# Performance work log

Measured on AMD Instinct MI355X. Metric: run time of the kernel, lower is better.

## Reference

```python
import jax, jax.numpy as jnp
import numpy as np

GROUP_SIZE = 128

def setup_inputs() -> dict:
    key = jax.random.key(0)
    k1, k2, k3, k4, k5 = jax.random.split(key, 5)
    B, S, IN, OUT = 4, 2048, 4096, 4096
    G = IN // GROUP_SIZE  # 32 groups
    x = jax.random.normal(k1, (B, S, IN), dtype=jnp.float32)
    qweight = jax.random.randint(k2, (OUT, IN // 2), 0, 256, dtype=jnp.int32)
    scales = jax.random.uniform(k3, (OUT, G), dtype=jnp.float32) * 0.01 + 1e-4
    zeros = jax.random.randint(k4, (OUT, G), 0, 16, dtype=jnp.int32)
    bias = jax.random.normal(k5, (OUT,), dtype=jnp.float32) * 0.01
    return {"x": x, "qweight": qweight, "scales": scales, "zeros": zeros, "bias": bias}

def reference(x, qweight, scales, zeros, bias):
    out_f, half = qweight.shape
    in_f = half * 2
    G = scales.shape[1]
    # Unpack two 4-bit values per byte: low nibble at even index, high at odd.
    low = (qweight & 15).astype(x.dtype)
    high = ((qweight >> 4) & 15).astype(x.dtype)
    w = jnp.stack([low, high], axis=-1).reshape(out_f, in_f)  # interleaved [w0,w1,w2,...]
    # Groupwise dequant: (q - zero) * scale
    w = w.reshape(out_f, G, GROUP_SIZE)
    w = (w - zeros[:, :, None].astype(x.dtype)) * scales[:, :, None].astype(x.dtype)
    w = w.reshape(out_f, in_f)
    # Dense linear: y = x @ W^T + b
    out = jnp.einsum('bsi,oi->bso', x, w) + bias
    return out
```

## Files before the change

kernel.cpp:

```cpp
#include <hip/hip_runtime.h>
#include <hip/hip_bf16.h>

typedef __attribute__((ext_vector_type(4))) float f32x4;
typedef __attribute__((ext_vector_type(8))) short bf16x8;
typedef __attribute__((ext_vector_type(4))) int i32x4;

#define GS 128

#define GLOAD_LDS16(g, l)                                                        \
    __builtin_amdgcn_global_load_lds(                                            \
        (const __attribute__((address_space(1))) void*)(g),                      \
        (__attribute__((address_space(3))) void*)(l), 16, 0, 0)

__device__ __forceinline__ short f2bf(float f) {
    union { float f; unsigned u; } v; v.f = f;
    unsigned r = v.u + 0x7fffu + ((v.u >> 16) & 1u);
    return (short)(r >> 16);
}

__global__ void requant_w_kernel(const int* __restrict__ QW,
                                 const float* __restrict__ SC,
                                 const int* __restrict__ ZR,
                                 signed char* __restrict__ W8,
                                 float* __restrict__ WS, int K, int G) {
    const int o = blockIdx.x;
    const int tid = threadIdx.x;
    const int lane = tid & 63;
    const int wid = tid >> 6;
    const int g = tid / 8;
    const float s = SC[(long)o * G + g];
    const float z = (float)ZR[(long)o * G + g];
    const int* p = QW + (long)o * (K / 2) + tid * 8;
    int v[8];
#pragma unroll
    for (int j = 0; j < 8; ++j) v[j] = p[j];
    float w[16];
#pragma unroll
    for (int j = 0; j < 8; ++j) {
        w[2 * j]     = ((float)(v[j] & 15) - z) * s;
        w[2 * j + 1] = ((float)((v[j] >> 4) & 15) - z) * s;
    }
    float am = 0.f;
#pragma unroll
    for (int j = 0; j < 16; ++j) am = fmaxf(am, fabsf(w[j]));
#pragma unroll
    for (int off = 32; off >= 1; off >>= 1) am = fmaxf(am, __shfl_xor(am, off));
    __shared__ float red[4];
    if (lane == 0) red[wid] = am;
    __syncthreads();
    float wmax = fmaxf(fmaxf(red[0], red[1]), fmaxf(red[2], red[3]));
    wmax = fmaxf(wmax, 1e-30f);
    const float qs = 127.0f / wmax;
    int out[4];
#pragma unroll
    for (int j = 0; j < 4; ++j) {
        int b0 = ((int)rintf(w[4 * j]     * qs)) & 255;
        int b1 = ((int)rintf(w[4 * j + 1] * qs)) & 255;
        int b2 = ((int)rintf(w[4 * j + 2] * qs)) & 255;
        int b3 = ((int)rintf(w[4 * j + 3] * qs)) & 255;
        out[j] = b0 | (b1 << 8) | (b2 << 16) | (b3 << 24);
    }
    *(i32x4*)(W8 + (long)o * K + tid * 16) = *(i32x4*)out;
    if (tid == 0) WS[o] = wmax / 127.0f;
}

__global__ void quant_x_kernel(const float* __restrict__ X,
                               signed char* __restrict__ Xq,
                               float* __restrict__ XS, int K) {
    const int row = blockIdx.x;
    const int tid = threadIdx.x;
    const int lane = tid & 63;
    const int wid = tid >> 6;
    const float* px = X + (long)row * K + tid * 16;
    f32x4 v[4];
#pragma unroll
    for (int j = 0; j < 4; ++j) v[j] = *(const f32x4*)(px + j * 4);
    float am = 0.f;
#pragma unroll
    for (int j = 0; j < 4; ++j)
#pragma unroll
        for (int i = 0; i < 4; ++i) am = fmaxf(am, fabsf(v[j][i]));
#pragma unroll
    for (int off = 32; off >= 1; off >>= 1) am = fmaxf(am, __shfl_xor(am, off));
    __shared__ float red[4];
    if (lane == 0) red[wid] = am;
    __syncthreads();
    float amax = fmaxf(fmaxf(red[0], red[1]), fmaxf(red[2], red[3]));
    amax = fmaxf(amax, 1e-30f);
    const float qs = 127.0f / amax;
    int out[4];
#pragma unroll
    for (int j = 0; j < 4; ++j) {
        int b0 = ((int)rintf(v[j][0] * qs)) & 255;
        int b1 = ((int)rintf(v[j][1] * qs)) & 255;
        int b2 = ((int)rintf(v[j][2] * qs)) & 255;
        int b3 = ((int)rintf(v[j][3] * qs)) & 255;
        out[j] = b0 | (b1 << 8) | (b2 << 16) | (b3 << 24);
    }
    *(i32x4*)(Xq + (long)row * K + tid * 16) = *(i32x4*)out;
    if (tid == 0) XS[row] = amax / 127.0f;
}

__global__ __launch_bounds__(512, 2)
void gemm_i8_kernel(const signed char* __restrict__ A,
                    const signed char* __restrict__ B,
                    const float* __restrict__ WS,
                    const float* __restrict__ XS,
                    const float* __restrict__ BI,
                    float* __restrict__ Y,
                    int M, int N, int K) {
    extern __shared__ char smem[];

    const int tid = threadIdx.x;
    const int lane = tid & 63;
    const int wid = tid >> 6;
    const int wr = wid >> 2;
    const int wc = wid & 3;
    const int fr = lane & 15;
    const int fq = lane >> 4;

    const int nbn = N / 256;
    const int bid = blockIdx.x;
    const int cpx = gridDim.x >> 3;
    const int wgid = (bid & 7) * cpx + (bid >> 3);
    const int tm = wgid / nbn;
    const int tn = wgid % nbn;
    const long m0 = (long)tm * 256;
    const long n0 = (long)tn * 256;

    const int srow = wid * 8 + (lane >> 3);
    const int schunk = (lane & 7) ^ (lane >> 3);
    const signed char* gA = A + (m0 + srow) * (long)K + schunk * 16;
    const signed char* gB = B + (n0 + srow) * (long)K + schunk * 16;

    auto stageA = [&](int c, int i, int kt) {
        GLOAD_LDS16(gA + (long)i * 64 * K + (long)kt * 128,
                    smem + c * 65536 + i * 8192 + wid * 1024);
    };
    auto stageB = [&](int c, int i, int kt) {
        GLOAD_LDS16(gB + (long)i * 64 * K + (long)kt * 128,
                    smem + c * 65536 + 32768 + i * 8192 + wid * 1024);
    };

    const int rswz = fr & 7;

    i32x4 acc[8][4] = {};
    i32x4 bfr[4][2];
    i32x4 afr[2][2];

    const int NT = K / 128;

    stageB(0, 0, 0); stageB(0, 1, 0); stageB(0, 2, 0); stageB(0, 3, 0);
    stageA(0, 0, 0); stageA(0, 2, 0);
    stageA(0, 1, 0); stageA(0, 3, 0);
    asm volatile("s_waitcnt vmcnt(2)" ::: "memory");
    __builtin_amdgcn_s_barrier();

    for (int t = 0; t < NT - 1; ++t) {
        const int cur = t & 1;
        const char* sA = smem + cur * 65536;
        const char* sB = sA + 32768;
        const int nxt = cur ^ 1;
#pragma unroll
        for (int q = 0; q < 4; ++q) {
#pragma unroll
            for (int ml = 0; ml < 2; ++ml)
#pragma unroll
                for (int ks = 0; ks < 2; ++ks) {
                    int row = wr * 128 + (2 * q + ml) * 16 + fr;
                    afr[ml][ks] = *(const i32x4*)(sA + row * 128 + ((fq + 4 * ks) ^ rswz) * 16);
                }
            if (q == 0) {
#pragma unroll
                for (int nf = 0; nf < 4; ++nf)
#pragma unroll
                    for (int ks = 0; ks < 2; ++ks) {
                        int row = wc * 64 + nf * 16 + fr;
                        bfr[nf][ks] = *(const i32x4*)(sB + row * 128 + ((fq + 4 * ks) ^ rswz) * 16);
                    }
            }
            if (q == 0)      { stageB(nxt, 0, t + 1); stageB(nxt, 1, t + 1); }
            else if (q == 1) { stageB(nxt, 2, t + 1); stageB(nxt, 3, t + 1); }
            else if (q == 2) { stageA(nxt, 0, t + 1); stageA(nxt, 2, t + 1); }
            else             { stageA(nxt, 1, t + 1); stageA(nxt, 3, t + 1); }

            if (q == 0) asm volatile("s_waitcnt lgkmcnt(8)" ::: "memory");
            __builtin_amdgcn_s_barrier();
            __builtin_amdgcn_s_setprio(1);
#pragma unroll
            for (int ml = 0; ml < 2; ++ml)
#pragma unroll
                for (int nf = 0; nf < 4; ++nf)
                    acc[2 * q + ml][nf] = __builtin_amdgcn_mfma_i32_16x16x64_i8(
                        afr[ml][0], bfr[nf][0], acc[2 * q + ml][nf], 0, 0, 0);
#pragma unroll
            for (int ml = 0; ml < 2; ++ml)
#pragma unroll
                for (int nf = 0; nf < 4; ++nf)
                    acc[2 * q + ml][nf] = __builtin_amdgcn_mfma_i32_16x16x64_i8(
                        afr[ml][1], bfr[nf][1], acc[2 * q + ml][nf], 0, 0, 0);
            __builtin_amdgcn_s_setprio(0);
            if (q == 1) asm volatile("s_waitcnt vmcnt(4)" ::: "memory");
            if (q == 3) asm volatile("s_waitcnt vmcnt(2)" ::: "memory");
            __builtin_amdgcn_s_barrier();
        }
    }

    {
        const int cur = (NT - 1) & 1;
        const char* sA = smem + cur * 65536;
        const char* sB = sA + 32768;
#pragma unroll
        for (int q = 0; q < 4; ++q) {
#pragma unroll
            for (int ml = 0; ml < 2; ++ml)
#pragma unroll
                for (int ks = 0; ks < 2; ++ks) {
                    int row = wr * 128 + (2 * q + ml) * 16 + fr;
                    afr[ml][ks] = *(const i32x4*)(sA + row * 128 + ((fq + 4 * ks) ^ rswz) * 16);
                }
            if (q == 0) {
#pragma unroll
                for (int nf = 0; nf < 4; ++nf)
#pragma unroll
                    for (int ks = 0; ks < 2; ++ks) {
                        int row = wc * 64 + nf * 16 + fr;
                        bfr[nf][ks] = *(const i32x4*)(sB + row * 128 + ((fq + 4 * ks) ^ rswz) * 16);
                    }
            }
            __builtin_amdgcn_s_barrier();
            __builtin_amdgcn_s_setprio(1);
#pragma unroll
            for (int ml = 0; ml < 2; ++ml)
#pragma unroll
                for (int nf = 0; nf < 4; ++nf)
                    acc[2 * q + ml][nf] = __builtin_amdgcn_mfma_i32_16x16x64_i8(
                        afr[ml][0], bfr[nf][0], acc[2 * q + ml][nf], 0, 0, 0);
#pragma unroll
            for (int ml = 0; ml < 2; ++ml)
#pragma unroll
                for (int nf = 0; nf < 4; ++nf)
                    acc[2 * q + ml][nf] = __builtin_amdgcn_mfma_i32_16x16x64_i8(
                        afr[ml][1], bfr[nf][1], acc[2 * q + ml][nf], 0, 0, 0);
            __builtin_amdgcn_s_setprio(0);
            if (q == 1) asm volatile("s_waitcnt vmcnt(0)" ::: "memory");
            __builtin_amdgcn_s_barrier();
        }
    }

#pragma unroll
    for (int nf = 0; nf < 4; ++nf) {
        const long col = n0 + wc * 64 + nf * 16 + fr;
        const float ws = WS[col];
        const float bv = BI[col];
#pragma unroll
        for (int m = 0; m < 8; ++m) {
            const long rbase = m0 + wr * 128 + m * 16 + 4 * fq;
#pragma unroll
            for (int i = 0; i < 4; ++i)
                Y[(rbase + i) * N + col] =
                    (float)acc[m][nf][i] * (XS[rbase + i] * ws) + bv;
        }
    }
}

#define BM 128
#define BN 128
#define BK 64
#define PK 72

__global__ void gptq_gemm_fallback(const float* __restrict__ X,
                                   const int* __restrict__ QW,
                                   const float* __restrict__ SC,
                                   const int* __restrict__ ZR,
                                   const float* __restrict__ BI,
                                   float* __restrict__ Y,
                                   int M, int N, int K, int G) {
    __shared__ __align__(16) short As[BM * PK];
    __shared__ __align__(16) short Bs[BN * PK];

    const int tid = threadIdx.x;
    const int nbm = M / BM;
    const int bid = blockIdx.x;
    const int cpx = gridDim.x >> 3;
    const int wgid = (bid & 7) * cpx + (bid >> 3);
    const int tm = wgid % nbm;
    const int tn = wgid / nbm;
    const long m0 = (long)tm * BM;
    const long n0 = (long)tn * BN;
    const int Kp = K >> 1;

    const int lane = tid & 63;
    const int wid = tid >> 6;
    const int wr = wid >> 1;
    const int wc = wid & 1;
    const int fr = lane & 15;
    const int fq = lane >> 4;

    int srow[4], sq[4];
#pragma unroll
    for (int c = 0; c < 4; ++c) {
        int w = tid + 256 * c;
        srow[c] = w >> 3;
        sq[c] = w & 7;
    }

    f32x4 acc[4][4] = {};
    const int NT = K / BK;

    for (int kt = 0; kt < NT; ++kt) {
        const int g = (kt * BK) / GS;
        f32x4 a0[4], a1[4];
        i32x4 b4[4];
        float sc_r[4], zr_r[4];
#pragma unroll
        for (int c = 0; c < 4; ++c) {
            const float* pa = X + (m0 + srow[c]) * K + kt * BK + 8 * sq[c];
            a0[c] = *(const f32x4*)pa;
            a1[c] = *(const f32x4*)(pa + 4);
            const int* pb = QW + (n0 + srow[c]) * Kp + kt * (BK / 2) + 4 * sq[c];
            b4[c] = *(const i32x4*)pb;
            sc_r[c] = SC[(n0 + srow[c]) * G + g];
            zr_r[c] = (float)ZR[(n0 + srow[c]) * G + g];
        }
        __syncthreads();
#pragma unroll
        for (int c = 0; c < 4; ++c) {
            bf16x8 av;
#pragma unroll
            for (int i = 0; i < 4; ++i) av[i] = f2bf(a0[c][i]);
#pragma unroll
            for (int i = 0; i < 4; ++i) av[4 + i] = f2bf(a1[c][i]);
            *(bf16x8*)(As + srow[c] * PK + 8 * sq[c]) = av;
            bf16x8 bv;
#pragma unroll
            for (int j = 0; j < 4; ++j) {
                int v = b4[c][j];
                bv[2 * j]     = f2bf(((float)(v & 15) - zr_r[c]) * sc_r[c]);
                bv[2 * j + 1] = f2bf(((float)((v >> 4) & 15) - zr_r[c]) * sc_r[c]);
            }
            *(bf16x8*)(Bs + srow[c] * PK + 8 * sq[c]) = bv;
        }
        __syncthreads();
#pragma unroll
        for (int kk = 0; kk < BK; kk += 32) {
            bf16x8 a[4], b[4];
#pragma unroll
            for (int mf = 0; mf < 4; ++mf)
                a[mf] = *(const bf16x8*)(As + (wr * 64 + mf * 16 + fr) * PK + kk + 8 * fq);
#pragma unroll
            for (int nf = 0; nf < 4; ++nf)
                b[nf] = *(const bf16x8*)(Bs + (wc * 64 + nf * 16 + fr) * PK + kk + 8 * fq);
#pragma unroll
            for (int mf = 0; mf < 4; ++mf)
#pragma unroll
                for (int nf = 0; nf < 4; ++nf)
                    acc[mf][nf] = __builtin_amdgcn_mfma_f32_16x16x32_bf16(
                        a[mf], b[nf], acc[mf][nf], 0, 0, 0);
        }
    }

#pragma unroll
    for (int nf = 0; nf < 4; ++nf) {
        const long col = n0 + wc * 64 + nf * 16 + fr;
        const float bias_v = BI[col];
#pragma unroll
        for (int mf = 0; mf < 4; ++mf) {
            const long rbase = m0 + wr * 64 + mf * 16 + 4 * fq;
#pragma unroll
            for (int i = 0; i < 4; ++i)
                Y[(rbase + i) * N + col] = acc[mf][nf][i] + bias_v;
        }
    }
}

extern "C" void kernel_launch(void* const* d_in, const int* in_sizes, int n_in,
                              void* d_out, int out_size, void* d_ws, size_t ws_size,
                              hipStream_t stream) {
    const float* X = (const float*)d_in[0];
    const int* QW = (const int*)d_in[1];
    const float* SC = (const float*)d_in[2];
    const int* ZR = (const int*)d_in[3];
    const float* BI = (const float*)d_in[4];
    float* Y = (float*)d_out;

    const int N = in_sizes[4];
    const int G = in_sizes[2] / N;
    const int K = G * GS;
    const int M = in_sizes[0] / K;

    const size_t needW8 = (size_t)N * K;
    const size_t needXq = (size_t)M * K;
    const size_t needXS = (size_t)M * 4;
    const size_t needWS = (size_t)N * 4;
    const size_t need = needW8 + needXq + needXS + needWS;

    if (ws_size >= need) {
        signed char* W8 = (signed char*)d_ws;
        signed char* Xq = W8 + needW8;
        float* XS = (float*)(Xq + needXq);
        float* WS = XS + M;

        hipLaunchKernelGGL(requant_w_kernel, dim3(N), dim3(256), 0, stream,
                           QW, SC, ZR, W8, WS, K, G);
        hipLaunchKernelGGL(quant_x_kernel, dim3(M), dim3(256), 0, stream,
                           X, Xq, XS, K);

        (void)hipFuncSetAttribute((const void*)gemm_i8_kernel,
                                  hipFuncAttributeMaxDynamicSharedMemorySize, 131072);
        const int grid = (M / 256) * (N / 256);
        hipLaunchKernelGGL(gemm_i8_kernel, dim3(grid), dim3(512), 131072, stream,
                           Xq, W8, WS, XS, BI, Y, M, N, K);
    } else {
        const int grid = (M / BM) * (N / BN);
        hipLaunchKernelGGL(gptq_gemm_fallback, dim3(grid), dim3(256), 0, stream,
                           X, QW, SC, ZR, BI, Y, M, N, K, G);
    }
}
```

Baseline: 185.9 us.

## Triple-buffer B tiles in int8 GEMM and merge quantization kernels

The GEMM now keeps three LDS buffers for the weight (B) tiles and two for the activation (A) tiles, raising dynamic shared memory to 160 KB. B tiles are prefetched two k-steps ahead, and an extra peeled iteration plus retuned vmcnt waits handle the deeper pipeline. The aim is to hide more global-load latency behind the MFMA work. Separately, the weight requantization and activation quantization kernels are merged into one launch with a block-index split, saving a launch and letting both jobs share the GPU. The larger LDS footprint uses nearly all of the per-CU LDS, and the hand-set waitcnt values must stay consistent with the new load order.

```diff
diff --git a/kernel.cpp b/kernel.cpp
--- a/kernel.cpp
+++ b/kernel.cpp
@@ -18,87 +18,86 @@
     return (short)(r >> 16);
 }
 
-__global__ void requant_w_kernel(const int* __restrict__ QW,
-                                 const float* __restrict__ SC,
-                                 const int* __restrict__ ZR,
-                                 signed char* __restrict__ W8,
-                                 float* __restrict__ WS, int K, int G) {
-    const int o = blockIdx.x;
+__global__ void prep_kernel(const int* __restrict__ QW,
+                            const float* __restrict__ SC,
+                            const int* __restrict__ ZR,
+                            const float* __restrict__ X,
+                            signed char* __restrict__ W8,
+                            float* __restrict__ WS,
+                            signed char* __restrict__ Xq,
+                            float* __restrict__ XS,
+                            int N, int K, int G) {
     const int tid = threadIdx.x;
     const int lane = tid & 63;
     const int wid = tid >> 6;
-    const int g = tid / 8;
-    const float s = SC[(long)o * G + g];
-    const float z = (float)ZR[(long)o * G + g];
-    const int* p = QW + (long)o * (K / 2) + tid * 8;
-    int v[8];
-#pragma unroll
-    for (int j = 0; j < 8; ++j) v[j] = p[j];
-    float w[16];
-#pragma unroll
-    for (int j = 0; j < 8; ++j) {
-        w[2 * j]     = ((float)(v[j] & 15) - z) * s;
-        w[2 * j + 1] = ((float)((v[j] >> 4) & 15) - z) * s;
-    }
-    float am = 0.f;
-#pragma unroll
-    for (int j = 0; j < 16; ++j) am = fmaxf(am, fabsf(w[j]));
-#pragma unroll
-    for (int off = 32; off >= 1; off >>= 1) am = fmaxf(am, __shfl_xor(am, off));
     __shared__ float red[4];
-    if (lane == 0) red[wid] = am;
-    __syncthreads();
-    float wmax = fmaxf(fmaxf(red[0], red[1]), fmaxf(red[2], red[3]));
-    wmax = fmaxf(wmax, 1e-30f);
-    const float qs = 127.0f / wmax;
-    int out[4];
-#pragma unroll
-    for (int j = 0; j < 4; ++j) {
-        int b0 = ((int)rintf(w[4 * j]     * qs)) & 255;
-        int b1 = ((int)rintf(w[4 * j + 1] * qs)) & 255;
-        int b2 = ((int)rintf(w[4 * j + 2] * qs)) & 255;
-        int b3 = ((int)rintf(w[4 * j + 3] * qs)) & 255;
-        out[j] = b0 | (b1 << 8) | (b2 << 16) | (b3 << 24);
-    }
-    *(i32x4*)(W8 + (long)o * K + tid * 16) = *(i32x4*)out;
-    if (tid == 0) WS[o] = wmax / 127.0f;
-}
-
-__global__ void quant_x_kernel(const float* __restrict__ X,
-                               signed char* __restrict__ Xq,
-                               float* __restrict__ XS, int K) {
-    const int row = blockIdx.x;
-    const int tid = threadIdx.x;
-    const int lane = tid & 63;
-    const int wid = tid >> 6;
-    const float* px = X + (long)row * K + tid * 16;
-    f32x4 v[4];
-#pragma unroll
-    for (int j = 0; j < 4; ++j) v[j] = *(const f32x4*)(px + j * 4);
-    float am = 0.f;
-#pragma unroll
-    for (int j = 0; j < 4; ++j)
-#pragma unroll
-        for (int i = 0; i < 4; ++i) am = fmaxf(am, fabsf(v[j][i]));
-#pragma unroll
-    for (int off = 32; off >= 1; off >>= 1) am = fmaxf(am, __shfl_xor(am, off));
-    __shared__ float red[4];
-    if (lane == 0) red[wid] = am;
-    __syncthreads();
-    float amax = fmaxf(fmaxf(red[0], red[1]), fmaxf(red[2], red[3]));
-    amax = fmaxf(amax, 1e-30f);
-    const float qs = 127.0f / amax;
-    int out[4];
-#pragma unroll
-    for (int j = 0; j < 4; ++j) {
-        int b0 = ((int)rintf(v[j][0] * qs)) & 255;
-        int b1 = ((int)rintf(v[j][1] * qs)) & 255;
-        int b2 = ((int)rintf(v[j][2] * qs)) & 255;
-        int b3 = ((int)rintf(v[j][3] * qs)) & 255;
-        out[j] = b0 | (b1 << 8) | (b2 << 16) | (b3 << 24);
-    }
-    *(i32x4*)(Xq + (long)row * K + tid * 16) = *(i32x4*)out;
-    if (tid == 0) XS[row] = amax / 127.0f;
+
+    if ((int)blockIdx.x < N) {
+        const int o = blockIdx.x;
+        const int g = tid / 8;
+        const float s = SC[(long)o * G + g];
+        const float z = (float)ZR[(long)o * G + g];
+        const int* p = QW + (long)o * (K / 2) + tid * 8;
+        int v[8];
+#pragma unroll
+        for (int j = 0; j < 8; ++j) v[j] = p[j];
+        float w[16];
+#pragma unroll
+        for (int j = 0; j < 8; ++j) {
+            w[2 * j]     = ((float)(v[j] & 15) - z) * s;
+            w[2 * j + 1] = ((float)((v[j] >> 4) & 15) - z) * s;
+        }
+        float am = 0.f;
+#pragma unroll
+        for (int j = 0; j < 16; ++j) am = fmaxf(am, fabsf(w[j]));
+#pragma unroll
+        for (int off = 32; off >= 1; off >>= 1) am = fmaxf(am, __shfl_xor(am, off));
+        if (lane == 0) red[wid] = am;
+        __syncthreads();
+        float wmax = fmaxf(fmaxf(red[0], red[1]), fmaxf(red[2], red[3]));
+        wmax = fmaxf(wmax, 1e-30f);
+        const float qs = 127.0f / wmax;
+        int out[4];
+#pragma unroll
+        for (int j = 0; j < 4; ++j) {
+            int b0 = ((int)rintf(w[4 * j]     * qs)) & 255;
+            int b1 = ((int)rintf(w[4 * j + 1] * qs)) & 255;
+            int b2 = ((int)rintf(w[4 * j + 2] * qs)) & 255;
+            int b3 = ((int)rintf(w[4 * j + 3] * qs)) & 255;
+            out[j] = b0 | (b1 << 8) | (b2 << 16) | (b3 << 24);
+        }
+        *(i32x4*)(W8 + (long)o * K + tid * 16) = *(i32x4*)out;
+        if (tid == 0) WS[o] = wmax / 127.0f;
+    } else {
+        const int row = blockIdx.x - N;
+        const float* px = X + (long)row * K + tid * 16;
+        f32x4 v[4];
+#pragma unroll
+        for (int j = 0; j < 4; ++j) v[j] = *(const f32x4*)(px + j * 4);
+        float am = 0.f;
+#pragma unroll
+        for (int j = 0; j < 4; ++j)
+#pragma unroll
+            for (int i = 0; i < 4; ++i) am = fmaxf(am, fabsf(v[j][i]));
+#pragma unroll
+        for (int off = 32; off >= 1; off >>= 1) am = fmaxf(am, __shfl_xor(am, off));
+        if (lane == 0) red[wid] = am;
+        __syncthreads();
+        float amax = fmaxf(fmaxf(red[0], red[1]), fmaxf(red[2], red[3]));
+        amax = fmaxf(amax, 1e-30f);
+        const float qs = 127.0f / amax;
+        int out[4];
+#pragma unroll
+        for (int j = 0; j < 4; ++j) {
+            int b0 = ((int)rintf(v[j][0] * qs)) & 255;
+            int b1 = ((int)rintf(v[j][1] * qs)) & 255;
+            int b2 = ((int)rintf(v[j][2] * qs)) & 255;
+            int b3 = ((int)rintf(v[j][3] * qs)) & 255;
+            out[j] = b0 | (b1 << 8) | (b2 << 16) | (b3 << 24);
+        }
+        *(i32x4*)(Xq + (long)row * K + tid * 16) = *(i32x4*)out;
+        if (tid == 0) XS[row] = amax / 127.0f;
+    }
 }
 
 __global__ __launch_bounds__(512, 2)
@@ -133,13 +132,13 @@
     const signed char* gA = A + (m0 + srow) * (long)K + schunk * 16;
     const signed char* gB = B + (n0 + srow) * (long)K + schunk * 16;
 
-    auto stageA = [&](int c, int i, int kt) {
+    auto stageA = [&](int c2, int i, int kt) {
         GLOAD_LDS16(gA + (long)i * 64 * K + (long)kt * 128,
-                    smem + c * 65536 + i * 8192 + wid * 1024);
+                    smem + c2 * 32768 + i * 8192 + wid * 1024);
     };
-    auto stageB = [&](int c, int i, int kt) {
+    auto stageB = [&](int b3, int i, int kt) {
         GLOAD_LDS16(gB + (long)i * 64 * K + (long)kt * 128,
-                    smem + c * 65536 + 32768 + i * 8192 + wid * 1024);
+                    smem + 65536 + b3 * 32768 + i * 8192 + wid * 1024);
     };
 
     const int rswz = fr & 7;
@@ -153,14 +152,15 @@
     stageB(0, 0, 0); stageB(0, 1, 0); stageB(0, 2, 0); stageB(0, 3, 0);
     stageA(0, 0, 0); stageA(0, 2, 0);
     stageA(0, 1, 0); stageA(0, 3, 0);
-    asm volatile("s_waitcnt vmcnt(2)" ::: "memory");
+    stageB(1, 0, 1); stageB(1, 1, 1); stageB(1, 2, 1); stageB(1, 3, 1);
+    asm volatile("s_waitcnt vmcnt(6)" ::: "memory");
     __builtin_amdgcn_s_barrier();
 
-    for (int t = 0; t < NT - 1; ++t) {
-        const int cur = t & 1;
-        const char* sA = smem + cur * 65536;
-        const char* sB = sA + 32768;
-        const int nxt = cur ^ 1;
+    for (int t = 0; t < NT - 2; ++t) {
+        const char* sA = smem + (t & 1) * 32768;
+        const char* sB = smem + 65536 + (t % 3) * 32768;
+        const int nxtA = (t & 1) ^ 1;
+        const int b2 = (t + 2) % 3;
 #pragma unroll
         for (int q = 0; q < 4; ++q) {
 #pragma unroll
@@ -179,10 +179,10 @@
                         bfr[nf][ks] = *(const i32x4*)(sB + row * 128 + ((fq + 4 * ks) ^ rswz) * 16);
                     }
             }
-            if (q == 0)      { stageB(nxt, 0, t + 1); stageB(nxt, 1, t + 1); }
-            else if (q == 1) { stageB(nxt, 2, t + 1); stageB(nxt, 3, t + 1); }
-            else if (q == 2) { stageA(nxt, 0, t + 1); stageA(nxt, 2, t + 1); }
-            else             { stageA(nxt, 1, t + 1); stageA(nxt, 3, t + 1); }
+            if (q == 0)      { stageA(nxtA, 0, t + 1); stageA(nxtA, 2, t + 1); }
+            else if (q == 1) { stageA(nxtA, 1, t + 1); stageA(nxtA, 3, t + 1); }
+            else if (q == 2) { stageB(b2, 0, t + 2); stageB(b2, 1, t + 2); }
+            else             { stageB(b2, 2, t + 2); stageB(b2, 3, t + 2); }
 
             if (q == 0) asm volatile("s_waitcnt lgkmcnt(8)" ::: "memory");
             __builtin_amdgcn_s_barrier();
@@ -200,16 +200,64 @@
                     acc[2 * q + ml][nf] = __builtin_amdgcn_mfma_i32_16x16x64_i8(
                         afr[ml][1], bfr[nf][1], acc[2 * q + ml][nf], 0, 0, 0);
             __builtin_amdgcn_s_setprio(0);
-            if (q == 1) asm volatile("s_waitcnt vmcnt(4)" ::: "memory");
+            if (q == 1) asm volatile("s_waitcnt vmcnt(8)" ::: "memory");
+            if (q == 3) asm volatile("s_waitcnt vmcnt(6)" ::: "memory");
+            __builtin_amdgcn_s_barrier();
+        }
+    }
+
+    {
+        const int t = NT - 2;
+        const char* sA = smem + (t & 1) * 32768;
+        const char* sB = smem + 65536 + (t % 3) * 32768;
+        const int nxtA = (t & 1) ^ 1;
+#pragma unroll
+        for (int q = 0; q < 4; ++q) {
+#pragma unroll
+            for (int ml = 0; ml < 2; ++ml)
+#pragma unroll
+                for (int ks = 0; ks < 2; ++ks) {
+                    int row = wr * 128 + (2 * q + ml) * 16 + fr;
+                    afr[ml][ks] = *(const i32x4*)(sA + row * 128 + ((fq + 4 * ks) ^ rswz) * 16);
+                }
+            if (q == 0) {
+#pragma unroll
+                for (int nf = 0; nf < 4; ++nf)
+#pragma unroll
+                    for (int ks = 0; ks < 2; ++ks) {
+                        int row = wc * 64 + nf * 16 + fr;
+                        bfr[nf][ks] = *(const i32x4*)(sB + row * 128 + ((fq + 4 * ks) ^ rswz) * 16);
+                    }
+            }
+            if (q == 0)      { stageA(nxtA, 0, t + 1); stageA(nxtA, 2, t + 1); }
+            else if (q == 1) { stageA(nxtA, 1, t + 1); stageA(nxtA, 3, t + 1); }
+
+            if (q == 0) asm volatile("s_waitcnt lgkmcnt(8)" ::: "memory");
+            __builtin_amdgcn_s_barrier();
+            __builtin_amdgcn_s_setprio(1);
+#pragma unroll
+            for (int ml = 0; ml < 2; ++ml)
+#pragma unroll
+                for (int nf = 0; nf < 4; ++nf)
+                    acc[2 * q + ml][nf] = __builtin_amdgcn_mfma_i32_16x16x64_i8(
+                        afr[ml][0], bfr[nf][0], acc[2 * q + ml][nf], 0, 0, 0);
+#pragma unroll
+            for (int ml = 0; ml < 2; ++ml)
+#pragma unroll
+                for (int nf = 0; nf < 4; ++nf)
+                    acc[2 * q + ml][nf] = __builtin_amdgcn_mfma_i32_16x16x64_i8(
+                        afr[ml][1], bfr[nf][1], acc[2 * q + ml][nf], 0, 0, 0);
+            __builtin_amdgcn_s_setprio(0);
+            if (q == 1) asm volatile("s_waitcnt vmcnt(8)" ::: "memory");
             if (q == 3) asm volatile("s_waitcnt vmcnt(2)" ::: "memory");
             __builtin_amdgcn_s_barrier();
         }
     }
 
     {
-        const int cur = (NT - 1) & 1;
-        const char* sA = smem + cur * 65536;
-        const char* sB = sA + 32768;
+        const int t = NT - 1;
+        const char* sA = smem + (t & 1) * 32768;
+        const char* sB = smem + 65536 + (t % 3) * 32768;
 #pragma unroll
         for (int q = 0; q < 4; ++q) {
 #pragma unroll
@@ -401,15 +449,13 @@
         float* XS = (float*)(Xq + needXq);
         float* WS = XS + M;
 
-        hipLaunchKernelGGL(requant_w_kernel, dim3(N), dim3(256), 0, stream,
-                           QW, SC, ZR, W8, WS, K, G);
-        hipLaunchKernelGGL(quant_x_kernel, dim3(M), dim3(256), 0, stream,
-                           X, Xq, XS, K);
+        hipLaunchKernelGGL(prep_kernel, dim3(N + M), dim3(256), 0, stream,
+                           QW, SC, ZR, X, W8, WS, Xq, XS, N, K, G);
 
         (void)hipFuncSetAttribute((const void*)gemm_i8_kernel,
-                                  hipFuncAttributeMaxDynamicSharedMemorySize, 131072);
+                                  hipFuncAttributeMaxDynamicSharedMemorySize, 163840);
         const int grid = (M / 256) * (N / 256);
-        hipLaunchKernelGGL(gemm_i8_kernel, dim3(grid), dim3(512), 131072, stream,
+        hipLaunchKernelGGL(gemm_i8_kernel, dim3(grid), dim3(512), 163840, stream,
                            Xq, W8, WS, XS, BI, Y, M, N, K);
     } else {
         const int grid = (M / BM) * (N / BN);
```

Measured after the change: 183.0 us. No clear change (-1.5%).
